# Performance work log

Hardware: AMD Instinct MI355X
Metric: run time of the kernel (lower is better)

The kernel has to match this reference:

```python
import jax, jax.numpy as jnp
import numpy as np
import math

B, S, D = 2, 4096, 1024
H, HD = 16, 64
R = 16

def _rope(x, cos, sin):
    # x: [B, S, H, HD]; cos/sin: [S, HD//2]
    xr = x.reshape(*x.shape[:-1], HD // 2, 2)
    xe, xo = xr[..., 0], xr[..., 1]
    c = cos[None, :, None, :]
    s = sin[None, :, None, :]
    # complex multiply (xe + i*xo) * (c + i*s)
    re = xe * c - xo * s
    im = xe * s + xo * c
    return jnp.stack([re, im], axis=-1).reshape(x.shape)

def setup_inputs() -> dict:
    key = jax.random.key(0)
    ks = jax.random.split(key, 20)
    inp = {}
    inp["x"] = jax.random.normal(ks[0], (B, S, D), dtype=jnp.float32)
    pos = jnp.arange(S, dtype=jnp.float32)
    inv_freq = 1.0 / (10000.0 ** (jnp.arange(0, HD, 2, dtype=jnp.float32) / HD))
    ang = pos[:, None] * inv_freq[None, :]  # [S, HD//2]
    inp["freqs_cos"] = jnp.cos(ang)
    inp["freqs_sin"] = jnp.sin(ang)
    causal = jnp.triu(jnp.full((S, S), -1e9, dtype=jnp.float32), k=1)
    inp["mask"] = causal[None, None, :, :]
    sc = 1.0 / math.sqrt(D)
    inp["wq_w"] = jax.random.normal(ks[1], (D, D), dtype=jnp.float32) * sc
    inp["wq_b"] = jnp.zeros((D,), dtype=jnp.float32)
    inp["wk_w"] = jax.random.normal(ks[2], (D, D), dtype=jnp.float32) * sc
    inp["wv_w"] = jax.random.normal(ks[3], (D, D), dtype=jnp.float32) * sc
    inp["wo_w"] = jax.random.normal(ks[4], (D, D), dtype=jnp.float32) * sc
    inp["wo_b"] = jnp.zeros((D,), dtype=jnp.float32)
    for i, nm in enumerate(["q", "k", "v", "o"]):
        inp[f"lora_{nm}_l1"] = jax.random.normal(ks[5 + 2 * i], (R, D), dtype=jnp.float32) * sc
        inp[f"lora_{nm}_l2"] = jax.random.normal(ks[6 + 2 * i], (D, R), dtype=jnp.float32) * 0.01
    return inp

def reference(x, freqs_cos, freqs_sin, mask, wq_w, wq_b, wk_w, wv_w, wo_w, wo_b,
              lora_q_l1, lora_q_l2, lora_k_l1, lora_k_l2,
              lora_v_l1, lora_v_l2, lora_o_l1, lora_o_l2):
    # QKV projections + LoRA deltas (torch Linear: y = x @ W.T + b, W is [out, in])
    xq = x @ wq_w.T + wq_b + (x @ lora_q_l1.T) @ lora_q_l2.T
    xk = x @ wk_w.T + (x @ lora_k_l1.T) @ lora_k_l2.T
    xv = x @ wv_w.T + (x @ lora_v_l1.T) @ lora_v_l2.T
    xq = xq.reshape(B, S, H, HD)
    xk = xk.reshape(B, S, H, HD)
    xv = xv.reshape(B, S, H, HD)
    xq = _rope(xq, freqs_cos, freqs_sin)
    xk = _rope(xk, freqs_cos, freqs_sin)
    # attention (training path: keys/values = current xk/xv, causal mask additive)
    scores = jnp.einsum('bqhd,bkhd->bhqk', xq, xk) / math.sqrt(HD)
    scores = scores + mask
    probs = jax.nn.softmax(scores.astype(jnp.float32), axis=-1).astype(xq.dtype)
    out = jnp.einsum('bhqk,bkhd->bqhd', probs, xv).reshape(B, S, D)
    return out @ wo_w.T + wo_b + (out @ lora_o_l1.T) @ lora_o_l2.T
```

## Files before the change

kernel.cpp:

```cpp
#include <hip/hip_runtime.h>
#include <hip/hip_bf16.h>
#include <stdint.h>

#define S_DIM 4096
#define D_DIM 1024
#define KAUG  1088
#define M_ROWS 8192

typedef short bf16x8 __attribute__((ext_vector_type(8)));
typedef float f32x4  __attribute__((ext_vector_type(4)));

__device__ __forceinline__ f32x4 mfma16(bf16x8 a, bf16x8 b, f32x4 c) {
  return __builtin_amdgcn_mfma_f32_16x16x32_bf16(a, b, c, 0, 0, 0);
}
__device__ __forceinline__ short f2bs(float f) {
  __hip_bfloat16 h = __float2bfloat16(f);
  return *reinterpret_cast<short*>(&h);
}
__device__ __forceinline__ short f2bs_fast(float f) {
  unsigned u = __builtin_bit_cast(unsigned, f) + 0x8000u;
  return (short)(u >> 16);
}
__device__ __forceinline__ unsigned pk2bf(float a, float b) {
  unsigned ua = __builtin_bit_cast(unsigned, a) + 0x8000u;
  unsigned ub = __builtin_bit_cast(unsigned, b) + 0x8000u;
  return __builtin_amdgcn_perm(ub, ua, 0x07060302);
}
__device__ __forceinline__ float bs2f(short s) {
  __hip_bfloat16 h;
  *reinterpret_cast<short*>(&h) = s;
  return __bfloat162float(h);
}
__device__ __forceinline__ float fexp2(float x) {
  return __builtin_amdgcn_exp2f(x);
}
__device__ __forceinline__ void gload16(const void* g, void* l) {
  __builtin_amdgcn_global_load_lds(
      (const __attribute__((address_space(1))) unsigned int*)g,
      (__attribute__((address_space(3))) unsigned int*)l, 16, 0, 0);
}

__global__ void prep_k(const float* __restrict__ x,
                       const float* __restrict__ wq, const float* __restrict__ wk,
                       const float* __restrict__ wv, const float* __restrict__ wo,
                       const float* __restrict__ wqb,
                       const float* __restrict__ lq1, const float* __restrict__ lq2,
                       const float* __restrict__ lk1, const float* __restrict__ lk2,
                       const float* __restrict__ lv1, const float* __restrict__ lv2,
                       const float* __restrict__ lo1, const float* __restrict__ lo2,
                       const float* __restrict__ cf, const float* __restrict__ sf,
                       short* __restrict__ xaug, short* __restrict__ wqkv,
                       short* __restrict__ woaug, short* __restrict__ l1cat,
                       float* __restrict__ biasc, float* __restrict__ cs2)
{
  unsigned i = blockIdx.x * 256u + threadIdx.x;
  if (i < 8388608u) {
    unsigned m = i >> 10, k = i & 1023u;
    xaug[(size_t)m * KAUG + k] = f2bs(x[i]);
    return;
  }
  i -= 8388608u;
  if (i < 3342336u) {
    unsigned n = i / 1088u, k = i - n * 1088u;
    float v;
    if (k < 1024u) {
      v = (n < 1024u) ? wq[n * 1024u + k]
        : (n < 2048u) ? wk[(n - 1024u) * 1024u + k]
                      : wv[(n - 2048u) * 1024u + k];
    } else {
      unsigned r = k - 1024u, blk = r >> 4, which = n >> 10;
      if (blk == which) {
        const float* l2 = which == 0 ? lq2 : which == 1 ? lk2 : lv2;
        v = l2[(n & 1023u) * 16u + (r & 15u)];
      } else v = 0.f;
    }
    wqkv[i] = f2bs(v);
    return;
  }
  i -= 3342336u;
  if (i < 1114112u) {
    unsigned n = i / 1088u, k = i - n * 1088u;
    float v = (k < 1024u) ? wo[n * 1024u + k]
            : (k < 1040u) ? lo2[n * 16u + (k - 1024u)] : 0.f;
    woaug[i] = f2bs(v);
    return;
  }
  i -= 1114112u;
  if (i < 65536u) {
    unsigned r = i >> 10, k = i & 1023u;
    const float* src = r < 16u ? lq1 : r < 32u ? lk1 : r < 48u ? lv1 : lo1;
    l1cat[i] = f2bs(src[(r & 15u) * 1024u + k]);
    return;
  }
  i -= 65536u;
  if (i < 3072u) {
    biasc[i] = (i < 1024u) ? wqb[i] : 0.f;
    return;
  }
  i -= 3072u;
  if (i < 131072u) {
    cs2[2u * i]     = cf[i];
    cs2[2u * i + 1] = sf[i];
  }
}

template<int MODE>
__global__ __launch_bounds__(256) void gemm_bt(
    const short* __restrict__ A, int lda,
    const short* __restrict__ B, int ldb,
    int N, int K,
    const float* __restrict__ bias,
    void* __restrict__ Cout, int ldc, int colofs,
    short* __restrict__ qo, short* __restrict__ ko, short* __restrict__ vo,
    const float* __restrict__ cs2)
{
  __shared__ short As[128 * 32];
  __shared__ short Bs[128 * 32];
  const int tid = threadIdx.x;
  const int w = tid >> 6, lane = tid & 63;
  const int q4 = lane >> 4, c = lane & 15;
  const int mh = w >> 1, nh = w & 1;
  const int mt = blockIdx.y, nt = blockIdx.x;

  const int rl = lane >> 2;
  const int kc = (lane & 3) * 8;

  const short* Ag0 = A + (size_t)(mt * 128 + w * 32 + rl) * lda + kc;
  const short* Ag1 = Ag0 + (size_t)16 * lda;
  int rb0 = nt * 128 + w * 32 + rl;      if (rb0 > N - 1) rb0 = N - 1;
  int rb1 = nt * 128 + w * 32 + 16 + rl; if (rb1 > N - 1) rb1 = N - 1;
  const short* Bg0 = B + (size_t)rb0 * ldb + kc;
  const short* Bg1 = B + (size_t)rb1 * ldb + kc;
  short* as0 = &As[(w * 32) * 32];
  short* as1 = &As[(w * 32 + 16) * 32];
  short* bs0 = &Bs[(w * 32) * 32];
  short* bs1 = &Bs[(w * 32 + 16) * 32];

  f32x4 acc[4][4];
#pragma unroll
  for (int ms = 0; ms < 4; ++ms)
#pragma unroll
    for (int ns = 0; ns < 4; ++ns) acc[ms][ns] = (f32x4){0.f, 0.f, 0.f, 0.f};

  const int nkt = K >> 5;
  for (int kt = 0; kt < nkt; ++kt) {
    __syncthreads();
    gload16(Ag0, as0);
    gload16(Ag1, as1);
    gload16(Bg0, bs0);
    gload16(Bg1, bs1);
    Ag0 += 32; Ag1 += 32; Bg0 += 32; Bg1 += 32;
    __syncthreads();
    bf16x8 af[4], bfr[4];
#pragma unroll
    for (int ms = 0; ms < 4; ++ms)
      af[ms] = *(const bf16x8*)&As[(mh * 64 + ms * 16 + c) * 32 + q4 * 8];
#pragma unroll
    for (int ns = 0; ns < 4; ++ns)
      bfr[ns] = *(const bf16x8*)&Bs[(nh * 64 + ns * 16 + c) * 32 + q4 * 8];
#pragma unroll
    for (int ms = 0; ms < 4; ++ms)
#pragma unroll
      for (int ns = 0; ns < 4; ++ns)
        acc[ms][ns] = mfma16(af[ms], bfr[ns], acc[ms][ns]);
  }

#pragma unroll
  for (int ms = 0; ms < 4; ++ms) {
#pragma unroll
    for (int ns = 0; ns < 4; ++ns) {
      const int n = nt * 128 + nh * 64 + ns * 16 + c;
      if (MODE == 0) {
        float bsv = (n < N) ? bias[n] : 0.f;
        float* Co = (float*)Cout;
#pragma unroll
        for (int r = 0; r < 4; ++r) {
          int m = mt * 128 + mh * 64 + ms * 16 + q4 * 4 + r;
          if (n < N) Co[(size_t)m * ldc + n] = acc[ms][ns][r] + bsv;
        }
      } else if (MODE == 1) {
        short* Co = (short*)Cout;
#pragma unroll
        for (int r = 0; r < 4; ++r) {
          int m = mt * 128 + mh * 64 + ms * 16 + q4 * 4 + r;
          if (n < N) Co[(size_t)m * ldc + colofs + n] = f2bs_fast(acc[ms][ns][r]);
        }
      } else {
        float bsv = bias[n];
        int which = n >> 10;
        int m0 = mt * 128 + mh * 64 + ms * 16 + q4 * 4;
        int bb = m0 >> 12, spos = m0 & 4095;
        if (which < 2) {
          int h = (n >> 6) & 15;
          int hd = n & 63;
          short* dst = which == 0 ? qo : ko;
          const float sgn = (c & 1) ? 1.f : -1.f;
          const int ihalf = hd >> 1;
#pragma unroll
          for (int r = 0; r < 4; ++r) {
            float val = acc[ms][ns][r] + bsv;
            float part = __shfl_xor(val, 1);
            float2 cs = *(const float2*)&cs2[((size_t)(spos + r) * 32 + ihalf) * 2];
            float res = val * cs.x + part * (sgn * cs.y);
            if (which == 0) res *= 0.18033688011112042f;
            dst[(size_t)((bb * 16 + h) * 4096 + spos + r) * 64 + hd] = f2bs_fast(res);
          }
        } else {
          int h = (n >> 6) & 15;
          int hd = n & 63;
          uint2 vk;
          vk.x = pk2bf(acc[ms][ns][0] + bsv, acc[ms][ns][1] + bsv);
          vk.y = pk2bf(acc[ms][ns][2] + bsv, acc[ms][ns][3] + bsv);
          *(uint2*)&vo[(((size_t)bb * 16 + h) * 64 + hd) * 4096 + spos] = vk;
        }
      }
    }
  }
}

template<int NT>
__global__ __launch_bounds__(256) void tgemm_k(
    const short* __restrict__ A, int lda,
    const short* __restrict__ B, int ldb,
    int N, int K, short* __restrict__ C, int ldc, int colofs)
{
  __shared__ short As[64 * 32];
  __shared__ short Bs[64 * 32];
  const int tid = threadIdx.x;
  const int w = tid >> 6, lane = tid & 63;
  const int q4 = lane >> 4, c = lane & 15;
  const int rl = lane >> 2, kc = (lane & 3) * 8;
  const int arow = w * 16 + rl;
  const int brow = arow <= N - 1 ? arow : N - 1;

  const short* Ag = A + (size_t)(blockIdx.x * 64 + arow) * lda + kc;
  const short* Bg = B + (size_t)brow * ldb + kc;
  short* asd = &As[(w * 16) * 32];
  short* bsd = &Bs[(w * 16) * 32];

  f32x4 acc[NT];
#pragma unroll
  for (int i = 0; i < NT; ++i) acc[i] = (f32x4){0.f, 0.f, 0.f, 0.f};

  const int nkt = K >> 5;
  for (int kt = 0; kt < nkt; ++kt) {
    __syncthreads();
    gload16(Ag, asd);
    gload16(Bg, bsd);
    Ag += 32; Bg += 32;
    __syncthreads();
    bf16x8 af = *(const bf16x8*)&As[(w * 16 + c) * 32 + q4 * 8];
#pragma unroll
    for (int nsi = 0; nsi < NT; ++nsi) {
      bf16x8 bf = *(const bf16x8*)&Bs[(nsi * 16 + c) * 32 + q4 * 8];
      acc[nsi] = mfma16(af, bf, acc[nsi]);
    }
  }
#pragma unroll
  for (int nsi = 0; nsi < NT; ++nsi) {
#pragma unroll
    for (int r = 0; r < 4; ++r) {
      int m = blockIdx.x * 64 + w * 16 + q4 * 4 + r;
      int n = nsi * 16 + c;
      if (n < N) C[(size_t)m * ldc + colofs + n] = f2bs_fast(acc[nsi][r]);
    }
  }
}

__global__ __launch_bounds__(256, 4) void flash_k(
    const short* __restrict__ Qb, const short* __restrict__ Kb,
    const short* __restrict__ Vt, short* __restrict__ Oaug)
{
  __shared__ short lds[20480];
  short* const PL = &lds[16384];

  const int id = (int)blockIdx.y * 32 + (int)blockIdx.x;
  const int g = id & 7, j = id >> 3;
  const int bh = g * 4 + (j >> 5);
  const int bx = j & 31;

  const int tid = threadIdx.x;
  const int w = tid >> 6, lane = tid & 63;
  const int q4 = lane >> 4, c = lane & 15;

  const short* Kg = Kb + (size_t)bh * 4096 * 64;
  const short* Vg = Vt + (size_t)bh * 64 * 4096;

  const int l8 = lane >> 3, l7 = lane & 7;
  const int sw = (l7 ^ l8) * 8;
  const int G0 = w * 2, G1 = w * 2 + 1;
  const int koff0 = (G0 * 8 + l8) * 64 + sw;
  const int koff1 = (G1 * 8 + l8) * 64 + sw;
  const int voff0 = (G0 * 8 + l8) * 4096 + sw;
  const int voff1 = (G1 * 8 + l8) * 4096 + sw;

  const int c7 = c & 7;
  const int chA0 = ((q4) ^ c7) * 8;
  const int chA1 = ((4 + q4) ^ c7) * 8;
  const int rowc = c * 64;
  const int rowq = (w * 16 + c) * 64;
  const int pw_base = (w * 16 + c) * 64 + (q4 & 1) * 4;
  const int pw_g = q4 >> 1;

  const int b = bh >> 4, h = bh & 15;

  for (int half = 0; half < 2; ++half) {
    const int qt = half == 0 ? 63 - bx : bx;
    const short* Qg = Qb + ((size_t)bh * 4096 + qt * 64) * 64;

    gload16(Qg + koff0, &lds[16384 + G0 * 512]);
    gload16(Qg + koff1, &lds[16384 + G1 * 512]);
    gload16(Kg + koff0, &lds[G0 * 512]);
    gload16(Kg + koff1, &lds[G1 * 512]);
    gload16(Vg + voff0, &lds[8192 + G0 * 512]);
    gload16(Vg + voff1, &lds[8192 + G1 * 512]);
    __syncthreads();

    bf16x8 qf0 = *(const bf16x8*)(PL + rowq + chA0);
    bf16x8 qf1 = *(const bf16x8*)(PL + rowq + chA1);

    f32x4 oacc[4];
#pragma unroll
    for (int i = 0; i < 4; ++i) oacc[i] = (f32x4){0.f, 0.f, 0.f, 0.f};
    float l_i = 0.f;

    for (int kt = 0; kt <= qt; ++kt) {
      const int cur = (kt & 1) * 4096;
      const short* Kc = &lds[cur];
      const short* Vc = &lds[8192 + cur];
      if (kt < qt) {
        const int nxt = ((kt + 1) & 1) * 4096;
        const short* ks = Kg + (size_t)(kt + 1) * 4096;
        const short* vs = Vg + (size_t)(kt + 1) * 64;
        gload16(ks + koff0, &lds[nxt + G0 * 512]);
        gload16(ks + koff1, &lds[nxt + G1 * 512]);
        gload16(vs + voff0, &lds[8192 + nxt + G0 * 512]);
        gload16(vs + voff1, &lds[8192 + nxt + G1 * 512]);
      }

      f32x4 st[4];
#pragma unroll
      for (int ns = 0; ns < 4; ++ns) {
        bf16x8 kf0 = *(const bf16x8*)(Kc + ns * 1024 + rowc + chA0);
        bf16x8 kf1 = *(const bf16x8*)(Kc + ns * 1024 + rowc + chA1);
        st[ns] = mfma16(kf0, qf0, (f32x4){0.f, 0.f, 0.f, 0.f});
        st[ns] = mfma16(kf1, qf1, st[ns]);
      }
      if (kt == qt) {
#pragma unroll
        for (int ns = 0; ns < 4; ++ns)
#pragma unroll
          for (int r = 0; r < 4; ++r)
            if (ns * 16 + q4 * 4 + r > w * 16 + c) st[ns][r] = -1e30f;
      }

      float ps[4][4];
#pragma unroll
      for (int ns = 0; ns < 4; ++ns)
#pragma unroll
        for (int r = 0; r < 4; ++r) ps[ns][r] = fexp2(st[ns][r]);

      float s0 = (ps[0][0] + ps[0][1]) + (ps[0][2] + ps[0][3]);
      float s1 = (ps[1][0] + ps[1][1]) + (ps[1][2] + ps[1][3]);
      float s2 = (ps[2][0] + ps[2][1]) + (ps[2][2] + ps[2][3]);
      float s3 = (ps[3][0] + ps[3][1]) + (ps[3][2] + ps[3][3]);
      float sum = (s0 + s1) + (s2 + s3);
      sum += __shfl_xor(sum, 16);
      sum += __shfl_xor(sum, 32);
      l_i += sum;

#pragma unroll
      for (int ns = 0; ns < 4; ++ns) {
        uint2 pk;
        pk.x = pk2bf(ps[ns][0], ps[ns][1]);
        pk.y = pk2bf(ps[ns][2], ps[ns][3]);
        *(uint2*)(PL + pw_base + (((ns * 2 + pw_g) ^ c7) * 8)) = pk;
      }
      bf16x8 pf0 = *(const bf16x8*)(PL + rowq + chA0);
      bf16x8 pf1 = *(const bf16x8*)(PL + rowq + chA1);

#pragma unroll
      for (int nc = 0; nc < 4; ++nc) {
        bf16x8 vf0 = *(const bf16x8*)(Vc + nc * 1024 + rowc + chA0);
        bf16x8 vf1 = *(const bf16x8*)(Vc + nc * 1024 + rowc + chA1);
        oacc[nc] = mfma16(vf0, pf0, oacc[nc]);
        oacc[nc] = mfma16(vf1, pf1, oacc[nc]);
      }
      __syncthreads();
    }

    float linv = 1.f / l_i;
#pragma unroll
    for (int nc = 0; nc < 4; ++nc) {
      uint2 ok;
      ok.x = pk2bf(oacc[nc][0] * linv, oacc[nc][1] * linv);
      ok.y = pk2bf(oacc[nc][2] * linv, oacc[nc][3] * linv);
      *(uint2*)(PL + pw_base + (((nc * 2 + pw_g) ^ c7) * 8)) = ok;
    }
    __syncthreads();
#pragma unroll
    for (int i2 = 0; i2 < 2; ++i2) {
      int ch = tid + i2 * 256;
      int r = ch >> 3, g2 = ch & 7;
      size_t row = (size_t)b * 4096 + qt * 64 + r;
      *(int4*)&Oaug[row * KAUG + h * 64 + g2 * 8] =
          *(const int4*)(PL + r * 64 + ((g2 ^ (r & 7)) * 8));
    }
    __syncthreads();
  }
}

extern "C" void kernel_launch(void* const* d_in, const int* in_sizes, int n_in,
                              void* d_out, int out_size, void* d_ws, size_t ws_size,
                              hipStream_t stream) {
  const float* x   = (const float*)d_in[0];
  const float* fc  = (const float*)d_in[1];
  const float* fs  = (const float*)d_in[2];
  const float* wq  = (const float*)d_in[4];
  const float* wqb = (const float*)d_in[5];
  const float* wk  = (const float*)d_in[6];
  const float* wv  = (const float*)d_in[7];
  const float* wo  = (const float*)d_in[8];
  const float* wob = (const float*)d_in[9];
  const float* lq1 = (const float*)d_in[10];
  const float* lq2 = (const float*)d_in[11];
  const float* lk1 = (const float*)d_in[12];
  const float* lk2 = (const float*)d_in[13];
  const float* lv1 = (const float*)d_in[14];
  const float* lv2 = (const float*)d_in[15];
  const float* lo1 = (const float*)d_in[16];
  const float* lo2 = (const float*)d_in[17];

  char* ws = (char*)d_ws;
  const size_t OFF_XAUG  = 0;
  const size_t OFF_XOAUG = 17825792;
  const size_t OFF_WQKV  = 35651584;
  const size_t OFF_WOAUG = 42336256;
  const size_t OFF_L1CAT = 44564480;
  const size_t OFF_BIASC = 44695552;
  const size_t OFF_QB    = 44707840;
  const size_t OFF_KB    = 61485056;
  const size_t OFF_VT    = 78262272;
  const size_t OFF_CS    = 95039488;

  short* xaug  = (short*)(ws + OFF_XAUG);
  short* xoaug = (short*)(ws + OFF_XOAUG);
  short* wqkv  = (short*)(ws + OFF_WQKV);
  short* woaug = (short*)(ws + OFF_WOAUG);
  short* l1cat = (short*)(ws + OFF_L1CAT);
  float* biasc = (float*)(ws + OFF_BIASC);
  short* qb    = (short*)(ws + OFF_QB);
  short* kb    = (short*)(ws + OFF_KB);
  short* vt    = (short*)(ws + OFF_VT);
  float* cs2   = (float*)(ws + OFF_CS);

  prep_k<<<50956, 256, 0, stream>>>(x, wq, wk, wv, wo, wqb,
                                    lq1, lq2, lk1, lk2, lv1, lv2, lo1, lo2,
                                    fc, fs,
                                    xaug, wqkv, woaug, l1cat, biasc, cs2);
  tgemm_k<3><<<128, 256, 0, stream>>>(xaug, KAUG, l1cat, 1024, 48, 1024,
                                      xaug, KAUG, 1024);
  gemm_bt<2><<<dim3(24, 64), 256, 0, stream>>>(xaug, KAUG, wqkv, KAUG, 3072, KAUG,
                                               biasc, nullptr, 0, 0, qb, kb, vt,
                                               cs2);
  flash_k<<<dim3(32, 32), 256, 0, stream>>>(qb, kb, vt, xoaug);
  tgemm_k<1><<<128, 256, 0, stream>>>(xoaug, KAUG, l1cat + 48 * 1024, 1024,
                                      16, 1024, xoaug, KAUG, 1024);
  gemm_bt<0><<<dim3(8, 64), 256, 0, stream>>>(xoaug, KAUG, woaug, KAUG, 1024, KAUG,
                                              wob, d_out, 1024, 0,
                                              nullptr, nullptr, nullptr, nullptr);
}
```

Measured before the change: 415.6 us.

## Process two 64-row query tiles per flash block to reuse K/V loads

The flash attention kernel now handles a 128-row query tile as two 64-row sub-tiles that share each staged K/V tile, halving the global K/V traffic and load instructions per query row. The grid shrinks to 16x32 blocks, LDS grows to hold a second P/Q buffer, and launch bounds drop to 2 blocks per CU to allow double the accumulators. In exchange it lowers occupancy and parallelism (512 blocks), and adds a wasted partially-masked diagonal iteration for the first sub-tile that is skipped by a branch.

Measured after the change: 404.4 us. 2.7% less time.

```diff
diff --git a/kernel.cpp b/kernel.cpp
--- a/kernel.cpp
+++ b/kernel.cpp
@@ -267,17 +267,17 @@
   }
 }
 
-__global__ __launch_bounds__(256, 4) void flash_k(
+__global__ __launch_bounds__(256, 2) void flash_k(
     const short* __restrict__ Qb, const short* __restrict__ Kb,
     const short* __restrict__ Vt, short* __restrict__ Oaug)
 {
-  __shared__ short lds[20480];
+  __shared__ short lds[24576];
   short* const PL = &lds[16384];
 
-  const int id = (int)blockIdx.y * 32 + (int)blockIdx.x;
+  const int id = (int)blockIdx.y * 16 + (int)blockIdx.x;
   const int g = id & 7, j = id >> 3;
-  const int bh = g * 4 + (j >> 5);
-  const int bx = j & 31;
+  const int bh = g * 4 + (j >> 4);
+  const int bx = j & 15;
 
   const int tid = threadIdx.x;
   const int w = tid >> 6, lane = tid & 63;
@@ -293,6 +293,11 @@
   const int koff1 = (G1 * 8 + l8) * 64 + sw;
   const int voff0 = (G0 * 8 + l8) * 4096 + sw;
   const int voff1 = (G1 * 8 + l8) * 4096 + sw;
+  const int qg = w * 4;
+  const int qoff0 = ((qg + 0) * 8 + l8) * 64 + sw;
+  const int qoff1 = ((qg + 1) * 8 + l8) * 64 + sw;
+  const int qoff2 = ((qg + 2) * 8 + l8) * 64 + sw;
+  const int qoff3 = ((qg + 3) * 8 + l8) * 64 + sw;
 
   const int c7 = c & 7;
   const int chA0 = ((q4) ^ c7) * 8;
@@ -305,30 +310,38 @@
   const int b = bh >> 4, h = bh & 15;
 
   for (int half = 0; half < 2; ++half) {
-    const int qt = half == 0 ? 63 - bx : bx;
-    const short* Qg = Qb + ((size_t)bh * 4096 + qt * 64) * 64;
-
-    gload16(Qg + koff0, &lds[16384 + G0 * 512]);
-    gload16(Qg + koff1, &lds[16384 + G1 * 512]);
+    const int qt = half == 0 ? 31 - bx : bx;
+    const short* Qg = Qb + ((size_t)bh * 4096 + qt * 128) * 64;
+
+    gload16(Qg + qoff0, &lds[16384 + (qg + 0) * 512]);
+    gload16(Qg + qoff1, &lds[16384 + (qg + 1) * 512]);
+    gload16(Qg + qoff2, &lds[16384 + (qg + 2) * 512]);
+    gload16(Qg + qoff3, &lds[16384 + (qg + 3) * 512]);
     gload16(Kg + koff0, &lds[G0 * 512]);
     gload16(Kg + koff1, &lds[G1 * 512]);
     gload16(Vg + voff0, &lds[8192 + G0 * 512]);
     gload16(Vg + voff1, &lds[8192 + G1 * 512]);
     __syncthreads();
 
-    bf16x8 qf0 = *(const bf16x8*)(PL + rowq + chA0);
-    bf16x8 qf1 = *(const bf16x8*)(PL + rowq + chA1);
-
-    f32x4 oacc[4];
-#pragma unroll
-    for (int i = 0; i < 4; ++i) oacc[i] = (f32x4){0.f, 0.f, 0.f, 0.f};
-    float l_i = 0.f;
-
-    for (int kt = 0; kt <= qt; ++kt) {
+    bf16x8 qa0 = *(const bf16x8*)(PL + rowq + chA0);
+    bf16x8 qa1 = *(const bf16x8*)(PL + rowq + chA1);
+    bf16x8 qb0 = *(const bf16x8*)(PL + 4096 + rowq + chA0);
+    bf16x8 qb1 = *(const bf16x8*)(PL + 4096 + rowq + chA1);
+
+    f32x4 oa[4], ob[4];
+#pragma unroll
+    for (int i = 0; i < 4; ++i) {
+      oa[i] = (f32x4){0.f, 0.f, 0.f, 0.f};
+      ob[i] = (f32x4){0.f, 0.f, 0.f, 0.f};
+    }
+    float la = 0.f, lb = 0.f;
+
+    const int last = 2 * qt + 1;
+    for (int kt = 0; kt <= last; ++kt) {
       const int cur = (kt & 1) * 4096;
       const short* Kc = &lds[cur];
       const short* Vc = &lds[8192 + cur];
-      if (kt < qt) {
+      if (kt < last) {
         const int nxt = ((kt + 1) & 1) * 4096;
         const short* ks = Kg + (size_t)(kt + 1) * 4096;
         const short* vs = Vg + (size_t)(kt + 1) * 64;
@@ -337,72 +350,115 @@
         gload16(vs + voff0, &lds[8192 + nxt + G0 * 512]);
         gload16(vs + voff1, &lds[8192 + nxt + G1 * 512]);
       }
-
-      f32x4 st[4];
+      const bool doA = (kt <= 2 * qt);
+
+      f32x4 sa[4], sb[4];
 #pragma unroll
       for (int ns = 0; ns < 4; ++ns) {
         bf16x8 kf0 = *(const bf16x8*)(Kc + ns * 1024 + rowc + chA0);
         bf16x8 kf1 = *(const bf16x8*)(Kc + ns * 1024 + rowc + chA1);
-        st[ns] = mfma16(kf0, qf0, (f32x4){0.f, 0.f, 0.f, 0.f});
-        st[ns] = mfma16(kf1, qf1, st[ns]);
-      }
-      if (kt == qt) {
+        sa[ns] = mfma16(kf0, qa0, (f32x4){0.f, 0.f, 0.f, 0.f});
+        sa[ns] = mfma16(kf1, qa1, sa[ns]);
+        sb[ns] = mfma16(kf0, qb0, (f32x4){0.f, 0.f, 0.f, 0.f});
+        sb[ns] = mfma16(kf1, qb1, sb[ns]);
+      }
+      if (kt == 2 * qt) {
 #pragma unroll
         for (int ns = 0; ns < 4; ++ns)
 #pragma unroll
           for (int r = 0; r < 4; ++r)
-            if (ns * 16 + q4 * 4 + r > w * 16 + c) st[ns][r] = -1e30f;
-      }
-
-      float ps[4][4];
-#pragma unroll
-      for (int ns = 0; ns < 4; ++ns)
-#pragma unroll
-        for (int r = 0; r < 4; ++r) ps[ns][r] = fexp2(st[ns][r]);
-
-      float s0 = (ps[0][0] + ps[0][1]) + (ps[0][2] + ps[0][3]);
-      float s1 = (ps[1][0] + ps[1][1]) + (ps[1][2] + ps[1][3]);
-      float s2 = (ps[2][0] + ps[2][1]) + (ps[2][2] + ps[2][3]);
-      float s3 = (ps[3][0] + ps[3][1]) + (ps[3][2] + ps[3][3]);
-      float sum = (s0 + s1) + (s2 + s3);
-      sum += __shfl_xor(sum, 16);
-      sum += __shfl_xor(sum, 32);
-      l_i += sum;
-
-#pragma unroll
-      for (int ns = 0; ns < 4; ++ns) {
-        uint2 pk;
-        pk.x = pk2bf(ps[ns][0], ps[ns][1]);
-        pk.y = pk2bf(ps[ns][2], ps[ns][3]);
-        *(uint2*)(PL + pw_base + (((ns * 2 + pw_g) ^ c7) * 8)) = pk;
-      }
-      bf16x8 pf0 = *(const bf16x8*)(PL + rowq + chA0);
-      bf16x8 pf1 = *(const bf16x8*)(PL + rowq + chA1);
+            if (ns * 16 + q4 * 4 + r > w * 16 + c) sa[ns][r] = -1e30f;
+      }
+      if (kt == last) {
+#pragma unroll
+        for (int ns = 0; ns < 4; ++ns)
+#pragma unroll
+          for (int r = 0; r < 4; ++r)
+            if (ns * 16 + q4 * 4 + r > w * 16 + c) sb[ns][r] = -1e30f;
+      }
+
+      bf16x8 pfa0, pfa1;
+      if (doA) {
+        float ps[4][4];
+#pragma unroll
+        for (int ns = 0; ns < 4; ++ns)
+#pragma unroll
+          for (int r = 0; r < 4; ++r) ps[ns][r] = fexp2(sa[ns][r]);
+        float s0 = (ps[0][0] + ps[0][1]) + (ps[0][2] + ps[0][3]);
+        float s1 = (ps[1][0] + ps[1][1]) + (ps[1][2] + ps[1][3]);
+        float s2 = (ps[2][0] + ps[2][1]) + (ps[2][2] + ps[2][3]);
+        float s3 = (ps[3][0] + ps[3][1]) + (ps[3][2] + ps[3][3]);
+        float sum = (s0 + s1) + (s2 + s3);
+        sum += __shfl_xor(sum, 16);
+        sum += __shfl_xor(sum, 32);
+        la += sum;
+#pragma unroll
+        for (int ns = 0; ns < 4; ++ns) {
+          uint2 pk;
+          pk.x = pk2bf(ps[ns][0], ps[ns][1]);
+          pk.y = pk2bf(ps[ns][2], ps[ns][3]);
+          *(uint2*)(PL + pw_base + (((ns * 2 + pw_g) ^ c7) * 8)) = pk;
+        }
+        pfa0 = *(const bf16x8*)(PL + rowq + chA0);
+        pfa1 = *(const bf16x8*)(PL + rowq + chA1);
+      }
+      {
+        float ps[4][4];
+#pragma unroll
+        for (int ns = 0; ns < 4; ++ns)
+#pragma unroll
+          for (int r = 0; r < 4; ++r) ps[ns][r] = fexp2(sb[ns][r]);
+        float s0 = (ps[0][0] + ps[0][1]) + (ps[0][2] + ps[0][3]);
+        float s1 = (ps[1][0] + ps[1][1]) + (ps[1][2] + ps[1][3]);
+        float s2 = (ps[2][0] + ps[2][1]) + (ps[2][2] + ps[2][3]);
+        float s3 = (ps[3][0] + ps[3][1]) + (ps[3][2] + ps[3][3]);
+        float sum = (s0 + s1) + (s2 + s3);
+        sum += __shfl_xor(sum, 16);
+        sum += __shfl_xor(sum, 32);
+        lb += sum;
+#pragma unroll
+        for (int ns = 0; ns < 4; ++ns) {
+          uint2 pk;
+          pk.x = pk2bf(ps[ns][0], ps[ns][1]);
+          pk.y = pk2bf(ps[ns][2], ps[ns][3]);
+          *(uint2*)(PL + 4096 + pw_base + (((ns * 2 + pw_g) ^ c7) * 8)) = pk;
+        }
+      }
+      bf16x8 pfb0 = *(const bf16x8*)(PL + 4096 + rowq + chA0);
+      bf16x8 pfb1 = *(const bf16x8*)(PL + 4096 + rowq + chA1);
 
 #pragma unroll
       for (int nc = 0; nc < 4; ++nc) {
         bf16x8 vf0 = *(const bf16x8*)(Vc + nc * 1024 + rowc + chA0);
         bf16x8 vf1 = *(const bf16x8*)(Vc + nc * 1024 + rowc + chA1);
-        oacc[nc] = mfma16(vf0, pf0, oacc[nc]);
-        oacc[nc] = mfma16(vf1, pf1, oacc[nc]);
+        if (doA) {
+          oa[nc] = mfma16(vf0, pfa0, oa[nc]);
+          oa[nc] = mfma16(vf1, pfa1, oa[nc]);
+        }
+        ob[nc] = mfma16(vf0, pfb0, ob[nc]);
+        ob[nc] = mfma16(vf1, pfb1, ob[nc]);
       }
       __syncthreads();
     }
 
-    float linv = 1.f / l_i;
+    float lia = 1.f / la, lib = 1.f / lb;
 #pragma unroll
     for (int nc = 0; nc < 4; ++nc) {
       uint2 ok;
-      ok.x = pk2bf(oacc[nc][0] * linv, oacc[nc][1] * linv);
-      ok.y = pk2bf(oacc[nc][2] * linv, oacc[nc][3] * linv);
+      ok.x = pk2bf(oa[nc][0] * lia, oa[nc][1] * lia);
+      ok.y = pk2bf(oa[nc][2] * lia, oa[nc][3] * lia);
       *(uint2*)(PL + pw_base + (((nc * 2 + pw_g) ^ c7) * 8)) = ok;
-    }
-    __syncthreads();
-#pragma unroll
-    for (int i2 = 0; i2 < 2; ++i2) {
+      uint2 ok2;
+      ok2.x = pk2bf(ob[nc][0] * lib, ob[nc][1] * lib);
+      ok2.y = pk2bf(ob[nc][2] * lib, ob[nc][3] * lib);
+      *(uint2*)(PL + 4096 + pw_base + (((nc * 2 + pw_g) ^ c7) * 8)) = ok2;
+    }
+    __syncthreads();
+#pragma unroll
+    for (int i2 = 0; i2 < 4; ++i2) {
       int ch = tid + i2 * 256;
       int r = ch >> 3, g2 = ch & 7;
-      size_t row = (size_t)b * 4096 + qt * 64 + r;
+      size_t row = (size_t)b * 4096 + qt * 128 + r;
       *(int4*)&Oaug[row * KAUG + h * 64 + g2 * 8] =
           *(const int4*)(PL + r * 64 + ((g2 ^ (r & 7)) * 8));
     }
@@ -463,7 +519,7 @@
   gemm_bt<2><<<dim3(24, 64), 256, 0, stream>>>(xaug, KAUG, wqkv, KAUG, 3072, KAUG,
                                                biasc, nullptr, 0, 0, qb, kb, vt,
                                                cs2);
-  flash_k<<<dim3(32, 32), 256, 0, stream>>>(qb, kb, vt, xoaug);
+  flash_k<<<dim3(16, 32), 256, 0, stream>>>(qb, kb, vt, xoaug);
   tgemm_k<1><<<128, 256, 0, stream>>>(xoaug, KAUG, l1cat + 48 * 1024, 1024,
                                       16, 1024, xoaug, KAUG, 1024);
   gemm_bt<0><<<dim3(8, 64), 256, 0, stream>>>(xoaug, KAUG, woaug, KAUG, 1024, KAUG,
```
